# Kernel optimization log

Hardware: AMD Instinct MI355X
Metric: run time of the kernel (lower is better)

Reference implementation:

```python
import jax, jax.numpy as jnp
import numpy as np

N_HEAD = 16
N_EMBED = 1024

def setup_inputs() -> dict:
    key = jax.random.key(0)
    ks = jax.random.split(key, 5)
    C = N_EMBED
    x = jax.random.normal(ks[0], (2, 2048, C), dtype=jnp.float32)
    # c_attn: Linear(C, 3C); c_proj: Linear(C, C). PyTorch Linear: y = x @ W.T + b
    w_attn = jax.random.normal(ks[1], (3 * C, C), dtype=jnp.float32) * (1.0 / np.sqrt(C))
    b_attn = jnp.zeros((3 * C,), dtype=jnp.float32)
    w_proj = jax.random.normal(ks[2], (C, C), dtype=jnp.float32) * (1.0 / np.sqrt(C))
    b_proj = jnp.zeros((C,), dtype=jnp.float32)
    return {"x": x, "w_attn": w_attn, "b_attn": b_attn, "w_proj": w_proj, "b_proj": b_proj}

def reference(x, w_attn, b_attn, w_proj, b_proj):
    B, T, C = x.shape
    H = N_HEAD
    D = C // H
    qkv = jnp.einsum('btc,fc->btf', x, w_attn) + b_attn  # [B,T,3C]
    q, k, v = jnp.split(qkv, 3, axis=-1)
    # [B,H,T,D]
    q = q.reshape(B, T, H, D).transpose(0, 2, 1, 3)
    k = k.reshape(B, T, H, D).transpose(0, 2, 1, 3)
    v = v.reshape(B, T, H, D).transpose(0, 2, 1, 3)
    att = jnp.einsum('bhqd,bhkd->bhqk', q, k) * (1.0 / np.sqrt(D))  # [B,H,T,T]
    causal = jnp.tril(jnp.ones((T, T), dtype=bool))
    att = jnp.where(causal[None, None], att, jnp.finfo(att.dtype).min)
    att = jax.nn.softmax(att, axis=-1)
    y = jnp.einsum('bhqk,bhkd->bhqd', att, v)  # [B,H,T,D]
    y = y.transpose(0, 2, 1, 3).reshape(B, T, C)
    return jnp.einsum('btc,fc->btf', y, w_proj) + b_proj
```

## Files before the change

kernel.cpp:

```cpp
#include <hip/hip_runtime.h>
#include <hip/hip_bf16.h>

typedef unsigned short u16;
typedef __attribute__((ext_vector_type(8))) short v8s;
typedef __attribute__((ext_vector_type(4))) short v4s;
typedef __attribute__((ext_vector_type(4))) float v4f;

#define SCL2 0.180336879f

__device__ __forceinline__ u16 f2bu(float f) {
  union { float f; unsigned u; } v; v.f = f;
  unsigned r = (v.u + 0x7fffu + ((v.u >> 16) & 1u)) >> 16;
  return (u16)r;
}
__device__ __forceinline__ v8s pack8(const v4f& a, const v4f& b) {
  union { v8s s; __hip_bfloat162 h[4]; } u;
  u.h[0] = __float22bfloat162_rn(make_float2(a[0], a[1]));
  u.h[1] = __float22bfloat162_rn(make_float2(a[2], a[3]));
  u.h[2] = __float22bfloat162_rn(make_float2(b[0], b[1]));
  u.h[3] = __float22bfloat162_rn(make_float2(b[2], b[3]));
  return u.s;
}

__device__ __forceinline__ void g2l16(const u16* g, u16* l) {
  __builtin_amdgcn_global_load_lds((const __attribute__((address_space(1))) void*)g,
                                   (__attribute__((address_space(3))) void*)l,
                                   16, 0, 0);
}

__global__ __launch_bounds__(256) void cvt_bf16(const float* __restrict__ s0, u16* __restrict__ d0, int n0,
                                                const float* __restrict__ s1, u16* __restrict__ d1, int n1,
                                                const float* __restrict__ s2, u16* __restrict__ d2, int n2) {
  int total8 = (n0 + n1 + n2) >> 3;
  for (int i = blockIdx.x * blockDim.x + threadIdx.x; i < total8; i += gridDim.x * blockDim.x) {
    int e = i << 3;
    const float* s; u16* d;
    if (e < n0)            { s = s0 + e;            d = d0 + e; }
    else if (e < n0 + n1)  { s = s1 + (e - n0);     d = d1 + (e - n0); }
    else                   { s = s2 + (e - n0 - n1); d = d2 + (e - n0 - n1); }
    v4f a = *(const v4f*)s, b = *(const v4f*)(s + 4);
    *(v8s*)d = pack8(a, b);
  }
}

__global__ __launch_bounds__(256) void gemm_qkv(const u16* __restrict__ A,
                                                const u16* __restrict__ W,
                                                const float* __restrict__ bias,
                                                u16* __restrict__ o0,
                                                u16* __restrict__ o1,
                                                u16* __restrict__ o2) {
  constexpr int K = 1024;
  __shared__ __align__(16) u16 As[128 * 64];
  __shared__ __align__(16) u16 Bs[128 * 64];
  const int tid = threadIdx.x;
  const int w = tid >> 6, lane = tid & 63, l15 = lane & 15, quad = lane >> 4;
  const int wm = w & 1, wn = w >> 1;
  const int R0 = blockIdx.x * 128, C0 = blockIdx.y * 128;

  v4f acc[4][4] = {};
  const u16* Ag = A + (size_t)R0 * K;
  const u16* Wg = W + (size_t)C0 * K;

  int srow[4], scol[4], sdst[4];
#pragma unroll
  for (int i = 0; i < 4; ++i) {
    int p = (w * 4 + i) * 64 + lane;
    srow[i] = p >> 3;
    scol[i] = (p & 7) * 8;
    sdst[i] = (w * 4 + i) * 512;
  }

  for (int k0 = 0; k0 < K; k0 += 64) {
    if (k0) __syncthreads();
#pragma unroll
    for (int i = 0; i < 4; ++i) g2l16(Ag + srow[i] * K + k0 + scol[i], &As[sdst[i]]);
#pragma unroll
    for (int i = 0; i < 4; ++i) g2l16(Wg + srow[i] * K + k0 + scol[i], &Bs[sdst[i]]);
    __syncthreads();
#pragma unroll
    for (int kk = 0; kk < 2; ++kk) {
      v8s a[4], b[4];
#pragma unroll
      for (int m = 0; m < 4; ++m)
        a[m] = *(const v8s*)&As[(wm * 64 + m * 16 + l15) * 64 + (kk * 4 + quad) * 8];
#pragma unroll
      for (int n = 0; n < 4; ++n)
        b[n] = *(const v8s*)&Bs[(wn * 64 + n * 16 + l15) * 64 + (kk * 4 + quad) * 8];
#pragma unroll
      for (int m = 0; m < 4; ++m)
#pragma unroll
        for (int n = 0; n < 4; ++n)
          acc[m][n] = __builtin_amdgcn_mfma_f32_16x16x32_bf16(a[m], b[n], acc[m][n], 0, 0, 0);
    }
  }

#pragma unroll
  for (int n = 0; n < 4; ++n) {
    int f = C0 + wn * 64 + n * 16 + l15;
    float bv = bias[f];
#pragma unroll
    for (int m = 0; m < 4; ++m) {
      int r0 = R0 + wm * 64 + m * 16 + quad * 4;
      int which = f >> 10, c = f & 1023;
      int h = c >> 6, d = c & 63;
      int b = r0 >> 11, t = r0 & 2047;
      if (which == 2) {
        v4s pk;
#pragma unroll
        for (int reg = 0; reg < 4; ++reg) pk[reg] = (short)f2bu(acc[m][n][reg] + bv);
        *(v4s*)&o2[(((b << 4) + h) * 64 + d) * 2048 + t] = pk;
      } else {
        u16* dst = (which == 0) ? o0 : o1;
        float sc = (which == 0) ? SCL2 : 1.0f;
#pragma unroll
        for (int reg = 0; reg < 4; ++reg)
          dst[(((b << 4) + h) * 2048 + (t + reg)) * 64 + d] = f2bu((acc[m][n][reg] + bv) * sc);
      }
    }
  }
}

__global__ __launch_bounds__(256) void gemm_proj(const u16* __restrict__ A,
                                                 const u16* __restrict__ W,
                                                 const float* __restrict__ bias,
                                                 float* __restrict__ out) {
  constexpr int K = 1024;
  __shared__ __align__(16) u16 As[128 * 64];
  __shared__ __align__(16) u16 Bs[64 * 64];
  const int tid = threadIdx.x;
  const int w = tid >> 6, lane = tid & 63, l15 = lane & 15, quad = lane >> 4;
  const int wm = w & 1, wn = w >> 1;
  const int R0 = blockIdx.x * 128, C0 = blockIdx.y * 64;

  v4f acc[4][2] = {};
  const u16* Ag = A + (size_t)R0 * K;
  const u16* Wg = W + (size_t)C0 * K;

  int arow[4], acol[4], adst[4];
#pragma unroll
  for (int i = 0; i < 4; ++i) {
    int p = (w * 4 + i) * 64 + lane;
    arow[i] = p >> 3; acol[i] = (p & 7) * 8; adst[i] = (w * 4 + i) * 512;
  }
  int brow[2], bcol[2], bdst[2];
#pragma unroll
  for (int i = 0; i < 2; ++i) {
    int p = (w * 2 + i) * 64 + lane;
    brow[i] = p >> 3; bcol[i] = (p & 7) * 8; bdst[i] = (w * 2 + i) * 512;
  }

  for (int k0 = 0; k0 < K; k0 += 64) {
    if (k0) __syncthreads();
#pragma unroll
    for (int i = 0; i < 4; ++i) g2l16(Ag + arow[i] * K + k0 + acol[i], &As[adst[i]]);
#pragma unroll
    for (int i = 0; i < 2; ++i) g2l16(Wg + brow[i] * K + k0 + bcol[i], &Bs[bdst[i]]);
    __syncthreads();
#pragma unroll
    for (int kk = 0; kk < 2; ++kk) {
      v8s a[4], b[2];
#pragma unroll
      for (int m = 0; m < 4; ++m)
        a[m] = *(const v8s*)&As[(wm * 64 + m * 16 + l15) * 64 + (kk * 4 + quad) * 8];
#pragma unroll
      for (int n = 0; n < 2; ++n)
        b[n] = *(const v8s*)&Bs[(wn * 32 + n * 16 + l15) * 64 + (kk * 4 + quad) * 8];
#pragma unroll
      for (int m = 0; m < 4; ++m)
#pragma unroll
        for (int n = 0; n < 2; ++n)
          acc[m][n] = __builtin_amdgcn_mfma_f32_16x16x32_bf16(a[m], b[n], acc[m][n], 0, 0, 0);
    }
  }

#pragma unroll
  for (int n = 0; n < 2; ++n) {
    int f = C0 + wn * 32 + n * 16 + l15;
    float bv = bias[f];
#pragma unroll
    for (int m = 0; m < 4; ++m) {
      int r0 = R0 + wm * 64 + m * 16 + quad * 4;
#pragma unroll
      for (int reg = 0; reg < 4; ++reg)
        out[(size_t)(r0 + reg) * 1024 + f] = acc[m][n][reg] + bv;
    }
  }
}

__global__ __launch_bounds__(256, 4) void attn_kernel(const u16* __restrict__ Q,
                                                      const u16* __restrict__ Kt,
                                                      const u16* __restrict__ Vt,
                                                      u16* __restrict__ Y) {
  __shared__ __align__(16) u16 Ksh[2][64 * 64], Vsh[2][64 * 64];
  const int tid = threadIdx.x;
  const int w = tid >> 6, lane = tid & 63, l15 = lane & 15, quad = lane >> 4;
  const int s = blockIdx.x, j = blockIdx.y;
  const int h = s & 15, p = s >> 4;
  const int b = j >> 1;
  const int qt = (j & 1) ? p : 31 - p;
  const int q0 = qt * 64 + w * 16;
  const int KT = qt + 1;
  const int bh = b * 16 + h;
  const u16* qg = Q + bh * 131072;
  const u16* kg = Kt + bh * 131072;
  const u16* vg = Vt + bh * 131072;

  v8s aq[2];
  {
    const u16* qr = qg + (q0 + l15) * 64;
    aq[0] = *(const v8s*)(qr + quad * 8);
    aq[1] = *(const v8s*)(qr + 32 + quad * 8);
  }

  v4f O[4] = {};
  float ll = 0.f;
  const int rowlim = w * 16 + l15;

  int ksg[2], kss[2], vsg[2], vs0[2], vs1[2];
#pragma unroll
  for (int i = 0; i < 2; ++i) {
    int srow = (tid >> 3) + i * 32, cc = tid & 7;
    ksg[i] = srow * 64 + cc * 8;
    kss[i] = srow * 64 + ((cc ^ (srow & 7)) * 8);
    vsg[i] = srow * 2048 + cc * 8;
    int vhi = cc >> 1, vlo = cc & 1;
    vs0[i] = srow * 64 + (((vhi * 2)     ^ (srow & 7)) * 8) + vlo * 4;
    vs1[i] = srow * 64 + (((vhi * 2 + 1) ^ (srow & 7)) * 8) + vlo * 4;
  }
  v8s tk[2], tv[2];
#pragma unroll
  for (int i = 0; i < 2; ++i) {
    tk[i] = *(const v8s*)(kg + ksg[i]);
    tv[i] = *(const v8s*)(vg + vsg[i]);
  }

  for (int kt = 0; kt < KT; ++kt) {
    const int buf = kt & 1;
#pragma unroll
    for (int i = 0; i < 2; ++i) {
      *(v8s*)&Ksh[buf][kss[i]] = tk[i];
      union { v8s v; v4s h[2]; } tvu; tvu.v = tv[i];
      *(v4s*)&Vsh[buf][vs0[i]] = tvu.h[0];
      *(v4s*)&Vsh[buf][vs1[i]] = tvu.h[1];
    }
    __syncthreads();
    if (kt + 1 < KT) {
      int kn = (kt + 1) * 64;
#pragma unroll
      for (int i = 0; i < 2; ++i) {
        tk[i] = *(const v8s*)(kg + kn * 64 + ksg[i]);
        tv[i] = *(const v8s*)(vg + kn + vsg[i]);
      }
    }
    const u16* Kb = Ksh[buf];
    const u16* Vb = Vsh[buf];

    v4f s4[4];
#pragma unroll
    for (int nt = 0; nt < 4; ++nt) {
      v4f z = {0.f, 0.f, 0.f, 0.f};
#pragma unroll
      for (int kk = 0; kk < 2; ++kk) {
        v8s kf = *(const v8s*)&Kb[(nt * 16 + l15) * 64 + (((kk * 4 + quad) ^ (l15 & 7)) * 8)];
        z = __builtin_amdgcn_mfma_f32_16x16x32_bf16(kf, aq[kk], z, 0, 0, 0);
      }
      s4[nt] = z;
    }

    float rs = 0.f;
    if (kt == qt) {
#pragma unroll
      for (int nt = 0; nt < 4; ++nt)
#pragma unroll
        for (int reg = 0; reg < 4; ++reg) {
          int kl = nt * 16 + quad * 4 + reg;
          float pv = (kl <= rowlim) ? exp2f(s4[nt][reg]) : 0.f;
          s4[nt][reg] = pv; rs += pv;
        }
    } else {
#pragma unroll
      for (int nt = 0; nt < 4; ++nt)
#pragma unroll
        for (int reg = 0; reg < 4; ++reg) {
          float pv = exp2f(s4[nt][reg]);
          s4[nt][reg] = pv; rs += pv;
        }
    }
    ll += rs;

    unsigned pk0[4], pk1[4];
#pragma unroll
    for (int nt = 0; nt < 4; ++nt) {
      union { __hip_bfloat162 h; unsigned u; } c0, c1;
      c0.h = __float22bfloat162_rn(make_float2(s4[nt][0], s4[nt][1]));
      c1.h = __float22bfloat162_rn(make_float2(s4[nt][2], s4[nt][3]));
      pk0[nt] = c0.u; pk1[nt] = c1.u;
    }
    asm volatile("v_permlane32_swap_b32 %0, %1" : "+v"(pk0[0]), "+v"(pk0[1]));
    asm volatile("v_permlane32_swap_b32 %0, %1" : "+v"(pk1[0]), "+v"(pk1[1]));
    asm volatile("v_permlane32_swap_b32 %0, %1" : "+v"(pk0[2]), "+v"(pk0[3]));
    asm volatile("v_permlane32_swap_b32 %0, %1" : "+v"(pk1[2]), "+v"(pk1[3]));
    v8s ap[2];
    {
      union { v8s v; unsigned u[4]; } a0, a1;
      a0.u[0] = pk0[0]; a0.u[1] = pk1[0]; a0.u[2] = pk0[1]; a0.u[3] = pk1[1];
      a1.u[0] = pk0[2]; a1.u[1] = pk1[2]; a1.u[2] = pk0[3]; a1.u[3] = pk1[3];
      ap[0] = a0.v; ap[1] = a1.v;
    }

#pragma unroll
    for (int nt = 0; nt < 4; ++nt)
#pragma unroll
      for (int kk = 0; kk < 2; ++kk) {
        v8s vf = *(const v8s*)&Vb[(nt * 16 + l15) * 64 + (((kk * 4 + quad) ^ (l15 & 7)) * 8)];
        O[nt] = __builtin_amdgcn_mfma_f32_16x16x32_bf16(ap[kk], vf, O[nt], 0, 0, 0);
      }
  }

  ll += __shfl_xor(ll, 16, 64); ll += __shfl_xor(ll, 32, 64);
  float li = 1.f / ll, lO[4];
#pragma unroll
  for (int reg = 0; reg < 4; ++reg) lO[reg] = __shfl(li, quad * 4 + reg, 64);
  const int tb = q0 + quad * 4;
#pragma unroll
  for (int nt = 0; nt < 4; ++nt)
#pragma unroll
    for (int reg = 0; reg < 4; ++reg)
      Y[(b * 2048 + tb + reg) * 1024 + h * 64 + nt * 16 + l15] = f2bu(O[nt][reg] * lO[reg]);
}

extern "C" void kernel_launch(void* const* d_in, const int* in_sizes, int n_in,
                              void* d_out, int out_size, void* d_ws, size_t ws_size,
                              hipStream_t stream) {
  const float* x      = (const float*)d_in[0];
  const float* w_attn = (const float*)d_in[1];
  const float* b_attn = (const float*)d_in[2];
  const float* w_proj = (const float*)d_in[3];
  const float* b_proj = (const float*)d_in[4];
  float* out = (float*)d_out;
  char* ws = (char*)d_ws;
  u16* xb  = (u16*)(ws);
  u16* wab = (u16*)(ws + (size_t)( 8u << 20));
  u16* wpb = (u16*)(ws + (size_t)(14u << 20));
  u16* q   = (u16*)(ws + (size_t)(16u << 20));
  u16* k   = (u16*)(ws + (size_t)(24u << 20));
  u16* vt  = (u16*)(ws + (size_t)(32u << 20));
  u16* y   = (u16*)(ws + (size_t)(40u << 20));

  cvt_bf16<<<2048, 256, 0, stream>>>(x, xb, 4194304, w_attn, wab, 3145728, w_proj, wpb, 1048576);
  gemm_qkv<<<dim3(32, 24), 256, 0, stream>>>(xb, wab, b_attn, q, k, vt);
  attn_kernel<<<dim3(256, 4), 256, 0, stream>>>(q, k, vt, y);
  gemm_proj<<<dim3(32, 16), 256, 0, stream>>>(y, wpb, b_proj, out);
}
```

Measured before the change: 177.2 us.

## Process 128-key tiles per iteration with single-buffered LDS in attention

The attention loop now stages 128 keys and values per iteration in one LDS buffer instead of double-buffering 64-key tiles, and processes two 64-key sub-tiles per barrier. This halves the number of loop iterations and the global-to-LDS round trips, which cuts the per-tile overhead. The cost is a second __syncthreads per iteration, since the buffer is no longer double-buffered. It also means twice the prefetch registers, and wasted loads of the masked second half when qt is even.

```diff
diff --git a/kernel.cpp b/kernel.cpp
--- a/kernel.cpp
+++ b/kernel.cpp
@@ -191,7 +191,8 @@
                                                       const u16* __restrict__ Kt,
                                                       const u16* __restrict__ Vt,
                                                       u16* __restrict__ Y) {
-  __shared__ __align__(16) u16 Ksh[2][64 * 64], Vsh[2][64 * 64];
+  __shared__ __align__(16) u16 Ksh[128 * 64];
+  __shared__ __align__(16) u16 Vsh[64 * 128];
   const int tid = threadIdx.x;
   const int w = tid >> 6, lane = tid & 63, l15 = lane & 15, quad = lane >> 4;
   const int s = blockIdx.x, j = blockIdx.y;
@@ -199,7 +200,7 @@
   const int b = j >> 1;
   const int qt = (j & 1) ? p : 31 - p;
   const int q0 = qt * 64 + w * 16;
-  const int KT = qt + 1;
+  const int NIT = (qt + 2) >> 1;
   const int bh = b * 16 + h;
   const u16* qg = Q + bh * 131072;
   const u16* kg = Kt + bh * 131072;
@@ -216,105 +217,111 @@
   float ll = 0.f;
   const int rowlim = w * 16 + l15;
 
-  int ksg[2], kss[2], vsg[2], vs0[2], vs1[2];
-#pragma unroll
-  for (int i = 0; i < 2; ++i) {
-    int srow = (tid >> 3) + i * 32, cc = tid & 7;
-    ksg[i] = srow * 64 + cc * 8;
-    kss[i] = srow * 64 + ((cc ^ (srow & 7)) * 8);
-    vsg[i] = srow * 2048 + cc * 8;
+  int ksg[4], kss[4], vsg[4], vv0[4], vv1[4];
+#pragma unroll
+  for (int i = 0; i < 4; ++i) {
+    int kr = (tid >> 3) + i * 32, kc = tid & 7;
+    ksg[i] = kr * 64 + kc * 8;
+    kss[i] = kr * 64 + ((kc ^ (kr & 7)) * 8);
+    int vr = (tid >> 4) + i * 16, c8 = tid & 15;
+    int half = c8 >> 3, cc = c8 & 7;
     int vhi = cc >> 1, vlo = cc & 1;
-    vs0[i] = srow * 64 + (((vhi * 2)     ^ (srow & 7)) * 8) + vlo * 4;
-    vs1[i] = srow * 64 + (((vhi * 2 + 1) ^ (srow & 7)) * 8) + vlo * 4;
-  }
-  v8s tk[2], tv[2];
-#pragma unroll
-  for (int i = 0; i < 2; ++i) {
+    vsg[i] = vr * 2048 + c8 * 8;
+    vv0[i] = vr * 128 + half * 64 + (((vhi * 2)     ^ (vr & 7)) * 8) + vlo * 4;
+    vv1[i] = vr * 128 + half * 64 + (((vhi * 2 + 1) ^ (vr & 7)) * 8) + vlo * 4;
+  }
+  v8s tk[4], tv[4];
+#pragma unroll
+  for (int i = 0; i < 4; ++i) {
     tk[i] = *(const v8s*)(kg + ksg[i]);
     tv[i] = *(const v8s*)(vg + vsg[i]);
   }
 
-  for (int kt = 0; kt < KT; ++kt) {
-    const int buf = kt & 1;
-#pragma unroll
-    for (int i = 0; i < 2; ++i) {
-      *(v8s*)&Ksh[buf][kss[i]] = tk[i];
-      union { v8s v; v4s h[2]; } tvu; tvu.v = tv[i];
-      *(v4s*)&Vsh[buf][vs0[i]] = tvu.h[0];
-      *(v4s*)&Vsh[buf][vs1[i]] = tvu.h[1];
+  for (int kt = 0; kt < NIT; ++kt) {
+#pragma unroll
+    for (int i = 0; i < 4; ++i) {
+      *(v8s*)&Ksh[kss[i]] = tk[i];
+      union { v8s v; v4s h2[2]; } u; u.v = tv[i];
+      *(v4s*)&Vsh[vv0[i]] = u.h2[0];
+      *(v4s*)&Vsh[vv1[i]] = u.h2[1];
     }
     __syncthreads();
-    if (kt + 1 < KT) {
-      int kn = (kt + 1) * 64;
-#pragma unroll
-      for (int i = 0; i < 2; ++i) {
+    if (kt + 1 < NIT) {
+      int kn = (kt + 1) * 128;
+#pragma unroll
+      for (int i = 0; i < 4; ++i) {
         tk[i] = *(const v8s*)(kg + kn * 64 + ksg[i]);
         tv[i] = *(const v8s*)(vg + kn + vsg[i]);
       }
     }
-    const u16* Kb = Ksh[buf];
-    const u16* Vb = Vsh[buf];
-
-    v4f s4[4];
-#pragma unroll
-    for (int nt = 0; nt < 4; ++nt) {
-      v4f z = {0.f, 0.f, 0.f, 0.f};
-#pragma unroll
-      for (int kk = 0; kk < 2; ++kk) {
-        v8s kf = *(const v8s*)&Kb[(nt * 16 + l15) * 64 + (((kk * 4 + quad) ^ (l15 & 7)) * 8)];
-        z = __builtin_amdgcn_mfma_f32_16x16x32_bf16(kf, aq[kk], z, 0, 0, 0);
+
+#pragma unroll
+    for (int ks = 0; ks < 2; ++ks) {
+      const int g = kt * 2 + ks;
+      if (g <= qt) {
+        v4f s4[4];
+#pragma unroll
+        for (int nt = 0; nt < 4; ++nt) {
+          v4f z = {0.f, 0.f, 0.f, 0.f};
+#pragma unroll
+          for (int kk = 0; kk < 2; ++kk) {
+            v8s kf = *(const v8s*)&Ksh[(ks * 64 + nt * 16 + l15) * 64 + (((kk * 4 + quad) ^ (l15 & 7)) * 8)];
+            z = __builtin_amdgcn_mfma_f32_16x16x32_bf16(kf, aq[kk], z, 0, 0, 0);
+          }
+          s4[nt] = z;
+        }
+
+        float rs = 0.f;
+        if (g == qt) {
+#pragma unroll
+          for (int nt = 0; nt < 4; ++nt)
+#pragma unroll
+            for (int reg = 0; reg < 4; ++reg) {
+              int kl = nt * 16 + quad * 4 + reg;
+              float pv = (kl <= rowlim) ? exp2f(s4[nt][reg]) : 0.f;
+              s4[nt][reg] = pv; rs += pv;
+            }
+        } else {
+#pragma unroll
+          for (int nt = 0; nt < 4; ++nt)
+#pragma unroll
+            for (int reg = 0; reg < 4; ++reg) {
+              float pv = exp2f(s4[nt][reg]);
+              s4[nt][reg] = pv; rs += pv;
+            }
+        }
+        ll += rs;
+
+        unsigned pk0[4], pk1[4];
+#pragma unroll
+        for (int nt = 0; nt < 4; ++nt) {
+          union { __hip_bfloat162 h; unsigned u; } c0, c1;
+          c0.h = __float22bfloat162_rn(make_float2(s4[nt][0], s4[nt][1]));
+          c1.h = __float22bfloat162_rn(make_float2(s4[nt][2], s4[nt][3]));
+          pk0[nt] = c0.u; pk1[nt] = c1.u;
+        }
+        asm volatile("v_permlane32_swap_b32 %0, %1" : "+v"(pk0[0]), "+v"(pk0[1]));
+        asm volatile("v_permlane32_swap_b32 %0, %1" : "+v"(pk1[0]), "+v"(pk1[1]));
+        asm volatile("v_permlane32_swap_b32 %0, %1" : "+v"(pk0[2]), "+v"(pk0[3]));
+        asm volatile("v_permlane32_swap_b32 %0, %1" : "+v"(pk1[2]), "+v"(pk1[3]));
+        v8s ap[2];
+        {
+          union { v8s v; unsigned u[4]; } a0, a1;
+          a0.u[0] = pk0[0]; a0.u[1] = pk1[0]; a0.u[2] = pk0[1]; a0.u[3] = pk1[1];
+          a1.u[0] = pk0[2]; a1.u[1] = pk1[2]; a1.u[2] = pk0[3]; a1.u[3] = pk1[3];
+          ap[0] = a0.v; ap[1] = a1.v;
+        }
+
+#pragma unroll
+        for (int nt = 0; nt < 4; ++nt)
+#pragma unroll
+          for (int kk = 0; kk < 2; ++kk) {
+            v8s vf = *(const v8s*)&Vsh[(nt * 16 + l15) * 128 + ks * 64 + (((kk * 4 + quad) ^ (l15 & 7)) * 8)];
+            O[nt] = __builtin_amdgcn_mfma_f32_16x16x32_bf16(ap[kk], vf, O[nt], 0, 0, 0);
+          }
       }
-      s4[nt] = z;
-    }
-
-    float rs = 0.f;
-    if (kt == qt) {
-#pragma unroll
-      for (int nt = 0; nt < 4; ++nt)
-#pragma unroll
-        for (int reg = 0; reg < 4; ++reg) {
-          int kl = nt * 16 + quad * 4 + reg;
-          float pv = (kl <= rowlim) ? exp2f(s4[nt][reg]) : 0.f;
-          s4[nt][reg] = pv; rs += pv;
-        }
-    } else {
-#pragma unroll
-      for (int nt = 0; nt < 4; ++nt)
-#pragma unroll
-        for (int reg = 0; reg < 4; ++reg) {
-          float pv = exp2f(s4[nt][reg]);
-          s4[nt][reg] = pv; rs += pv;
-        }
-    }
-    ll += rs;
-
-    unsigned pk0[4], pk1[4];
-#pragma unroll
-    for (int nt = 0; nt < 4; ++nt) {
-      union { __hip_bfloat162 h; unsigned u; } c0, c1;
-      c0.h = __float22bfloat162_rn(make_float2(s4[nt][0], s4[nt][1]));
-      c1.h = __float22bfloat162_rn(make_float2(s4[nt][2], s4[nt][3]));
-      pk0[nt] = c0.u; pk1[nt] = c1.u;
-    }
-    asm volatile("v_permlane32_swap_b32 %0, %1" : "+v"(pk0[0]), "+v"(pk0[1]));
-    asm volatile("v_permlane32_swap_b32 %0, %1" : "+v"(pk1[0]), "+v"(pk1[1]));
-    asm volatile("v_permlane32_swap_b32 %0, %1" : "+v"(pk0[2]), "+v"(pk0[3]));
-    asm volatile("v_permlane32_swap_b32 %0, %1" : "+v"(pk1[2]), "+v"(pk1[3]));
-    v8s ap[2];
-    {
-      union { v8s v; unsigned u[4]; } a0, a1;
-      a0.u[0] = pk0[0]; a0.u[1] = pk1[0]; a0.u[2] = pk0[1]; a0.u[3] = pk1[1];
-      a1.u[0] = pk0[2]; a1.u[1] = pk1[2]; a1.u[2] = pk0[3]; a1.u[3] = pk1[3];
-      ap[0] = a0.v; ap[1] = a1.v;
-    }
-
-#pragma unroll
-    for (int nt = 0; nt < 4; ++nt)
-#pragma unroll
-      for (int kk = 0; kk < 2; ++kk) {
-        v8s vf = *(const v8s*)&Vb[(nt * 16 + l15) * 64 + (((kk * 4 + quad) ^ (l15 & 7)) * 8)];
-        O[nt] = __builtin_amdgcn_mfma_f32_16x16x32_bf16(ap[kk], vf, O[nt], 0, 0, 0);
-      }
+    }
+    if (kt + 1 < NIT) __syncthreads();
   }
 
   ll += __shfl_xor(ll, 16, 64); ll += __shfl_xor(ll, 32, 64);
```

Result: slower. 241.7 us (+36.4%).
